# Kernel tuning notes

Measured on AMD Instinct MI355X. Metric: run time of the kernel, lower is better.

The kernel has to match this reference:

```python
import jax, jax.numpy as jnp
import numpy as np

C_IN = 128
C_HID = 32
N_HEAD = 4
LN_EPS = 1e-5


def layer_norm(x, w, b):
    mu = jnp.mean(x, axis=-1, keepdims=True)
    var = jnp.mean(jnp.square(x - mu), axis=-1, keepdims=True)
    return (x - mu) * jax.lax.rsqrt(var + LN_EPS) * w + b


def setup_inputs() -> dict:
    key = jax.random.key(0)
    ks = jax.random.split(key, 12)
    B, N = 1, 256
    act = jax.random.normal(ks[0], (B, N, N, C_IN), dtype=jnp.float32)
    mask = jnp.ones((B, N, N), dtype=jnp.float32)
    s_in = 1.0 / np.sqrt(C_IN)
    s_o = 1.0 / np.sqrt(C_HID * N_HEAD)
    return {
        "act": act,
        "mask": mask,
        "ln_w": jnp.ones((C_IN,), jnp.float32),
        "ln_b": jnp.zeros((C_IN,), jnp.float32),
        "w_2d": jax.random.normal(ks[1], (C_IN, N_HEAD), jnp.float32) * s_in,
        "wq": jax.random.normal(ks[2], (C_IN, N_HEAD * C_HID), jnp.float32) * s_in,
        "wk": jax.random.normal(ks[3], (C_IN, N_HEAD * C_HID), jnp.float32) * s_in,
        "wv": jax.random.normal(ks[4], (C_IN, N_HEAD * C_HID), jnp.float32) * s_in,
        "wg": jax.random.normal(ks[5], (C_IN, N_HEAD * C_HID), jnp.float32) * s_in,
        "bg": jnp.ones((N_HEAD * C_HID,), jnp.float32),
        "wo": jax.random.normal(ks[6], (N_HEAD * C_HID, C_IN), jnp.float32) * s_o,
        "bo": jnp.zeros((C_IN,), jnp.float32),
    }


def reference(act, mask, ln_w, ln_b, w_2d, wq, wk, wv, wg, bg, wo, bo):
    B, N = act.shape[0], act.shape[1]
    H, c = N_HEAD, C_HID

    x = layer_norm(act, ln_w, ln_b)                       # [B,I,J,C]

    # mask bias: [B, I, 1, 1, K]
    bias = (1e9 * (mask - 1.0))[:, :, None, None, :]
    # pair bias from projected activations: [B, 1, H, Q, K]
    nb = jnp.einsum("bqkc,ch->bhqk", x, w_2d)[:, None]

    scale = c ** (-0.5)
    q = (x @ wq).reshape(B, N, N, H, c) * scale           # [B,I,Q,H,c]
    k = (x @ wk).reshape(B, N, N, H, c)                   # [B,I,K,H,c]
    v = (x @ wv).reshape(B, N, N, H, c)

    logits = jnp.einsum("biqhc,bikhc->bihqk", q, k) + bias + nb
    a = jax.nn.softmax(logits, axis=-1)                   # [B,I,H,Q,K]
    o = jnp.einsum("bihqk,bikhc->biqhc", a, v)            # [B,I,Q,H,c]

    g = jax.nn.sigmoid(x @ wg + bg).reshape(B, N, N, H, c)
    o = (o * g).reshape(B, N, N, H * c)
    return o @ wo + bo
```

## Files before the change

### kernel.cpp

```cpp
#include <hip/hip_runtime.h>
#include <hip/hip_bf16.h>
#include <math.h>

#define C_IN   128
#define NSEQ   256
#define LN_EPS 1e-5f
#define LOG2E  1.4426950408889634f

typedef __attribute__((ext_vector_type(8))) short bf16x8;
typedef __attribute__((ext_vector_type(4))) float f32x4;

__device__ __forceinline__ short f2bf(float x) {
    unsigned u = __builtin_bit_cast(unsigned, x);
    u = (u + 0x7FFF + ((u >> 16) & 1)) >> 16;
    return (short)u;
}


__global__ __launch_bounds__(256) void prep_kernel(
    const float* __restrict__ wq, const float* __restrict__ wk,
    const float* __restrict__ wv, const float* __restrict__ wg,
    const float* __restrict__ wo, const float* __restrict__ w2d,
    short* __restrict__ wT)
{
    int gid = blockIdx.x * 256 + threadIdx.x;
    if (gid < 5 * 16384) {
        int m = gid >> 14, r = gid & 16383, col = r >> 7, k = r & 127;
        const float* W = (m == 0) ? wq : (m == 1) ? wk : (m == 2) ? wv
                       : (m == 3) ? wg : wo;
        float s = (m == 0) ? (0.17677669529663687f * LOG2E) : 1.0f;
        wT[gid] = f2bf(W[k * 128 + col] * s);
    } else if (gid < 5 * 16384 + 16 * 128) {
        int r = gid - 5 * 16384, col = r >> 7, k = r & 127;
        float v = (col < 4) ? w2d[k * 4 + col] * LOG2E : 0.0f;
        wT[gid] = f2bf(v);
    }
}

__global__ __launch_bounds__(256) void proj_kernel(
    const float* __restrict__ act, const float* __restrict__ ln_w,
    const float* __restrict__ ln_b, const float* __restrict__ bg,
    const short* __restrict__ wT,
    short* __restrict__ q_buf, short* __restrict__ k_buf,
    short* __restrict__ v_buf, float* __restrict__ g_buf,
    float* __restrict__ nb2)
{
    __shared__ float psum[4][64], psq[4][64];
    __shared__ float mu_s[64], rs_s[64];
    __shared__ float lnw_s[128], lnb_s[128];

    const int tid = threadIdx.x;
    const int pbase = blockIdx.x * 64;

    if (tid < 128) { lnw_s[tid] = ln_w[tid]; lnb_s[tid] = ln_b[tid]; }

    {
        int m = tid >> 2, qd = tid & 3;
        const float* row = act + (size_t)(pbase + m) * 128 + qd * 32;
        float a = 0.f, b = 0.f;
        #pragma unroll
        for (int j = 0; j < 8; ++j) {
            float4 t = *(const float4*)(row + j * 4);
            a += t.x + t.y + t.z + t.w;
            b += t.x * t.x + t.y * t.y + t.z * t.z + t.w * t.w;
        }
        psum[qd][m] = a; psq[qd][m] = b;
    }
    __syncthreads();
    if (tid < 64) {
        float a = psum[0][tid] + psum[1][tid] + psum[2][tid] + psum[3][tid];
        float b = psq[0][tid] + psq[1][tid] + psq[2][tid] + psq[3][tid];
        float mu = a * (1.f / 128.f);
        float var = b * (1.f / 128.f) - mu * mu;
        mu_s[tid] = mu; rs_s[tid] = rsqrtf(var + LN_EPS);
    }
    __syncthreads();

    const int w = tid >> 6, l = tid & 63, lr = l & 15, lh = l >> 4;

    bf16x8 af[4][4];
    #pragma unroll
    for (int qt = 0; qt < 4; ++qt) {
        int m = qt * 16 + lr;
        float mu = mu_s[m], rs = rs_s[m];
        const float* rowp = act + (size_t)(pbase + m) * 128 + lh * 8;
        #pragma unroll
        for (int kc = 0; kc < 4; ++kc) {
            float4 a = *(const float4*)(rowp + kc * 32);
            float4 b = *(const float4*)(rowp + kc * 32 + 4);
            int c0 = kc * 32 + lh * 8;
            bf16x8 f;
            f[0] = f2bf((a.x - mu) * rs * lnw_s[c0 + 0] + lnb_s[c0 + 0]);
            f[1] = f2bf((a.y - mu) * rs * lnw_s[c0 + 1] + lnb_s[c0 + 1]);
            f[2] = f2bf((a.z - mu) * rs * lnw_s[c0 + 2] + lnb_s[c0 + 2]);
            f[3] = f2bf((a.w - mu) * rs * lnw_s[c0 + 3] + lnb_s[c0 + 3]);
            f[4] = f2bf((b.x - mu) * rs * lnw_s[c0 + 4] + lnb_s[c0 + 4]);
            f[5] = f2bf((b.y - mu) * rs * lnw_s[c0 + 5] + lnb_s[c0 + 5]);
            f[6] = f2bf((b.z - mu) * rs * lnw_s[c0 + 6] + lnb_s[c0 + 6]);
            f[7] = f2bf((b.w - mu) * rs * lnw_s[c0 + 7] + lnb_s[c0 + 7]);
            af[qt][kc] = f;
        }
    }

    const int nct = (w == 0) ? 9 : 8;
    for (int ct = 0; ct < nct; ++ct) {
        const short* bp = (ct < 8)
            ? (wT + w * 16384 + (ct * 16 + lr) * 128 + lh * 8)
            : (wT + 5 * 16384 + lr * 128 + lh * 8);
        f32x4 z = {0.f, 0.f, 0.f, 0.f};
        f32x4 acc0 = z, acc1 = z, acc2 = z, acc3 = z;
        #pragma unroll
        for (int kc = 0; kc < 4; ++kc) {
            bf16x8 b = *(const bf16x8*)(bp + kc * 32);
            acc0 = __builtin_amdgcn_mfma_f32_16x16x32_bf16(af[0][kc], b, acc0, 0, 0, 0);
            acc1 = __builtin_amdgcn_mfma_f32_16x16x32_bf16(af[1][kc], b, acc1, 0, 0, 0);
            acc2 = __builtin_amdgcn_mfma_f32_16x16x32_bf16(af[2][kc], b, acc2, 0, 0, 0);
            acc3 = __builtin_amdgcn_mfma_f32_16x16x32_bf16(af[3][kc], b, acc3, 0, 0, 0);
        }
        f32x4 acc[4] = {acc0, acc1, acc2, acc3};
        if (ct < 8) {
            int col = ct * 16 + lr;
            if (w == 3) {
                float bgv = bg[col];
                #pragma unroll
                for (int qt = 0; qt < 4; ++qt)
                    #pragma unroll
                    for (int r = 0; r < 4; ++r) {
                        float v = acc[qt][r] + bgv;
                        v = 1.f / (1.f + exp2f(-v * LOG2E));
                        g_buf[(size_t)(pbase + qt * 16 + lh * 4 + r) * 128 + col] = v;
                    }
            } else {
                short* obuf = (w == 0) ? q_buf : (w == 1) ? k_buf : v_buf;
                #pragma unroll
                for (int qt = 0; qt < 4; ++qt)
                    #pragma unroll
                    for (int r = 0; r < 4; ++r)
                        obuf[(size_t)(pbase + qt * 16 + lh * 4 + r) * 128 + col] =
                            f2bf(acc[qt][r]);
            }
        } else {
            int col = lr;
            if (col < 4) {
                #pragma unroll
                for (int qt = 0; qt < 4; ++qt)
                    #pragma unroll
                    for (int r = 0; r < 4; ++r)
                        nb2[(size_t)col * 65536 + pbase + qt * 16 + lh * 4 + r] =
                            acc[qt][r];
            }
        }
    }
}

__global__ __launch_bounds__(256) void attn_kernel(
    const float* __restrict__ mask,
    const short* __restrict__ q_buf, const short* __restrict__ k_buf,
    const short* __restrict__ v_buf, const float* __restrict__ g_buf,
    const float* __restrict__ nb2, short* __restrict__ og_buf)
{
    __shared__ short k_s[256 * 40];
    __shared__ short vt_s[32 * 264];
    __shared__ short p_s[4][64 * 40];
    __shared__ float bias_s[256];

    const int tid = threadIdx.x, bid = blockIdx.x;
    const int i = bid >> 2, h = bid & 3;
    const size_t pb = (size_t)i * 256 * 128 + h * 32;

    {
        const short* kp = k_buf + pb + (size_t)tid * 128;
        const short* vp = v_buf + pb + (size_t)tid * 128;
        bf16x8 kv[4], vv[4];
        #pragma unroll
        for (int j = 0; j < 4; ++j) kv[j] = *(const bf16x8*)(kp + j * 8);
        #pragma unroll
        for (int j = 0; j < 4; ++j) vv[j] = *(const bf16x8*)(vp + j * 8);
        #pragma unroll
        for (int j = 0; j < 4; ++j) *(bf16x8*)&k_s[tid * 40 + j * 8] = kv[j];
        #pragma unroll
        for (int j = 0; j < 4; ++j)
            #pragma unroll
            for (int e = 0; e < 8; ++e)
                vt_s[(j * 8 + e) * 264 + tid] = vv[j][e];
        bias_s[tid] = 1e9f * (mask[i * 256 + tid] - 1.f) * LOG2E;
    }

    const int w = tid >> 6, l = tid & 63, lr = l & 15, lh = l >> 4;
    const int qbase = w * 64;

    bf16x8 qf[4];
    #pragma unroll
    for (int qt = 0; qt < 4; ++qt)
        qf[qt] = *(const bf16x8*)(q_buf + pb +
                    (size_t)(qbase + qt * 16 + lr) * 128 + lh * 8);
    __syncthreads();

    f32x4 z = {0.f, 0.f, 0.f, 0.f};
    f32x4 o[4][2];
    float lsum[4][4];
    #pragma unroll
    for (int qt = 0; qt < 4; ++qt) {
        o[qt][0] = z; o[qt][1] = z;
        #pragma unroll
        for (int r = 0; r < 4; ++r) lsum[qt][r] = 0.f;
    }
    short* pw = &p_s[w][0];

    for (int kk = 0; kk < 256; kk += 32) {
        bf16x8 bk0 = *(const bf16x8*)&k_s[(kk + lr) * 40 + lh * 8];
        bf16x8 bk1 = *(const bf16x8*)&k_s[(kk + 16 + lr) * 40 + lh * 8];
        f32x4 s[4][2];
        #pragma unroll
        for (int qt = 0; qt < 4; ++qt) {
            s[qt][0] = __builtin_amdgcn_mfma_f32_16x16x32_bf16(qf[qt], bk0, z, 0, 0, 0);
            s[qt][1] = __builtin_amdgcn_mfma_f32_16x16x32_bf16(qf[qt], bk1, z, 0, 0, 0);
        }
        float b0 = bias_s[kk + lr], b1 = bias_s[kk + 16 + lr];
        #pragma unroll
        for (int qt = 0; qt < 4; ++qt) {
            int q = qbase + qt * 16 + lh * 4;
            const float* nbp = nb2 + (size_t)h * 65536 + (size_t)q * 256 + kk + lr;
            #pragma unroll
            for (int r = 0; r < 4; ++r) {
                float n0 = nbp[r * 256], n1 = nbp[r * 256 + 16];
                float p0 = exp2f(s[qt][0][r] + b0 + n0);
                float p1 = exp2f(s[qt][1][r] + b1 + n1);
                lsum[qt][r] += p0 + p1;
                pw[(qt * 16 + lh * 4 + r) * 40 + lr]      = f2bf(p0);
                pw[(qt * 16 + lh * 4 + r) * 40 + 16 + lr] = f2bf(p1);
            }
        }
        __syncthreads();
        bf16x8 bv0 = *(const bf16x8*)&vt_s[lr * 264 + kk + lh * 8];
        bf16x8 bv1 = *(const bf16x8*)&vt_s[(16 + lr) * 264 + kk + lh * 8];
        #pragma unroll
        for (int qt = 0; qt < 4; ++qt) {
            bf16x8 ap = *(const bf16x8*)&pw[(qt * 16 + lr) * 40 + lh * 8];
            o[qt][0] = __builtin_amdgcn_mfma_f32_16x16x32_bf16(ap, bv0, o[qt][0], 0, 0, 0);
            o[qt][1] = __builtin_amdgcn_mfma_f32_16x16x32_bf16(ap, bv1, o[qt][1], 0, 0, 0);
        }
        __syncthreads();
    }

    #pragma unroll
    for (int qt = 0; qt < 4; ++qt)
        #pragma unroll
        for (int r = 0; r < 4; ++r) {
            float v = lsum[qt][r];
            v += __shfl_xor(v, 1); v += __shfl_xor(v, 2);
            v += __shfl_xor(v, 4); v += __shfl_xor(v, 8);
            lsum[qt][r] = 1.f / v;
        }

    #pragma unroll
    for (int qt = 0; qt < 4; ++qt)
        #pragma unroll
        for (int ct = 0; ct < 2; ++ct) {
            int c = ct * 16 + lr;
            #pragma unroll
            for (int r = 0; r < 4; ++r) {
                int q = qbase + qt * 16 + lh * 4 + r;
                size_t idx = pb + (size_t)q * 128 + c;
                float gv = g_buf[idx];
                og_buf[idx] = f2bf(o[qt][ct][r] * lsum[qt][r] * gv);
            }
        }
}

__global__ __launch_bounds__(256) void out_kernel(
    const short* __restrict__ og_buf, const short* __restrict__ wT,
    const float* __restrict__ bo, float* __restrict__ out)
{
    const int tid = threadIdx.x;
    const int pbase = blockIdx.x * 64;
    const int w = tid >> 6, l = tid & 63, lr = l & 15, lh = l >> 4;

    bf16x8 af[4][4];
    #pragma unroll
    for (int qt = 0; qt < 4; ++qt) {
        const short* rp = og_buf + (size_t)(pbase + qt * 16 + lr) * 128 + lh * 8;
        #pragma unroll
        for (int kc = 0; kc < 4; ++kc) af[qt][kc] = *(const bf16x8*)(rp + kc * 32);
    }
    const short* wo_t = wT + 4 * 16384;
    f32x4 z = {0.f, 0.f, 0.f, 0.f};
    #pragma unroll
    for (int ct = 0; ct < 2; ++ct) {
        int col = w * 32 + ct * 16 + lr;
        f32x4 acc0 = z, acc1 = z, acc2 = z, acc3 = z;
        #pragma unroll
        for (int kc = 0; kc < 4; ++kc) {
            bf16x8 b = *(const bf16x8*)(wo_t + col * 128 + kc * 32 + lh * 8);
            acc0 = __builtin_amdgcn_mfma_f32_16x16x32_bf16(af[0][kc], b, acc0, 0, 0, 0);
            acc1 = __builtin_amdgcn_mfma_f32_16x16x32_bf16(af[1][kc], b, acc1, 0, 0, 0);
            acc2 = __builtin_amdgcn_mfma_f32_16x16x32_bf16(af[2][kc], b, acc2, 0, 0, 0);
            acc3 = __builtin_amdgcn_mfma_f32_16x16x32_bf16(af[3][kc], b, acc3, 0, 0, 0);
        }
        f32x4 acc[4] = {acc0, acc1, acc2, acc3};
        float bov = bo[col];
        #pragma unroll
        for (int qt = 0; qt < 4; ++qt)
            #pragma unroll
            for (int r = 0; r < 4; ++r)
                out[(size_t)(pbase + qt * 16 + lh * 4 + r) * 128 + col] =
                    acc[qt][r] + bov;
    }
}

extern "C" void kernel_launch(void* const* d_in, const int* in_sizes, int n_in,
                              void* d_out, int out_size, void* d_ws, size_t ws_size,
                              hipStream_t stream) {
    const float* act  = (const float*)d_in[0];
    const float* mask = (const float*)d_in[1];
    const float* ln_w = (const float*)d_in[2];
    const float* ln_b = (const float*)d_in[3];
    const float* w2d  = (const float*)d_in[4];
    const float* wq   = (const float*)d_in[5];
    const float* wk   = (const float*)d_in[6];
    const float* wv   = (const float*)d_in[7];
    const float* wg   = (const float*)d_in[8];
    const float* bg   = (const float*)d_in[9];
    const float* wo   = (const float*)d_in[10];
    const float* bo   = (const float*)d_in[11];
    float* out = (float*)d_out;

    char* ws = (char*)d_ws;
    short* q_buf  = (short*)(ws);
    short* k_buf  = (short*)(ws + 16777216);
    short* v_buf  = (short*)(ws + 2 * 16777216);
    short* og_buf = (short*)(ws + 3 * 16777216);
    float* g_buf  = (float*)(ws + 4 * 16777216);
    float* nb2    = (float*)(ws + 4 * 16777216 + 33554432);
    short* wT     = (short*)(ws + 4 * 16777216 + 33554432 + 1048576);

    prep_kernel<<<328, 256, 0, stream>>>(wq, wk, wv, wg, wo, w2d, wT);
    proj_kernel<<<1024, 256, 0, stream>>>(act, ln_w, ln_b, bg, wT,
                                          q_buf, k_buf, v_buf, g_buf, nb2);
    attn_kernel<<<1024, 256, 0, stream>>>(mask, q_buf, k_buf, v_buf, g_buf,
                                          nb2, og_buf);
    out_kernel<<<1024, 256, 0, stream>>>(og_buf, wT, bo, out);
}
```

Measured before the change: 130.8 us.

## Restructure projection/attention: transposed V, bf16 gate, LDS-staged coalesced stores, no K/V LDS

The projection kernel now handles 32 rows per block across twice as many blocks. Its outputs are staged through LDS so global stores are coalesced, V is written pre-transposed, and the gate is stored as bf16 instead of fp32. The attention kernel drops its K/V LDS staging and per-iteration barriers, reading K and transposed V straight from global memory, and packs probabilities with a hardware bf16 convert. The aim is less memory traffic and fewer syncs, at the cost of more global loads inside the attention inner loop and some gate precision.

```diff
diff --git a/kernel.cpp b/kernel.cpp
--- a/kernel.cpp
+++ b/kernel.cpp
@@ -1,19 +1,20 @@
 #include <hip/hip_runtime.h>
-#include <hip/hip_bf16.h>
 #include <math.h>
 
-#define C_IN   128
-#define NSEQ   256
+#define LOG2E  1.4426950408889634f
 #define LN_EPS 1e-5f
-#define LOG2E  1.4426950408889634f
 
 typedef __attribute__((ext_vector_type(8))) short bf16x8;
 typedef __attribute__((ext_vector_type(4))) float f32x4;
+typedef __attribute__((ext_vector_type(4))) unsigned u32x4;
 
 __device__ __forceinline__ short f2bf(float x) {
     unsigned u = __builtin_bit_cast(unsigned, x);
     u = (u + 0x7FFF + ((u >> 16) & 1)) >> 16;
     return (short)u;
+}
+__device__ __forceinline__ float bf2f(unsigned short b) {
+    return __builtin_bit_cast(float, (unsigned)b << 16);
 }
 
 
@@ -42,45 +43,45 @@
     const float* __restrict__ ln_b, const float* __restrict__ bg,
     const short* __restrict__ wT,
     short* __restrict__ q_buf, short* __restrict__ k_buf,
-    short* __restrict__ v_buf, float* __restrict__ g_buf,
+    short* __restrict__ v_t, short* __restrict__ g_buf,
     float* __restrict__ nb2)
 {
-    __shared__ float psum[4][64], psq[4][64];
-    __shared__ float mu_s[64], rs_s[64];
+    __shared__ short trans[4][32 * 136];
+    __shared__ float mu_s[32], rs_s[32];
     __shared__ float lnw_s[128], lnb_s[128];
 
     const int tid = threadIdx.x;
-    const int pbase = blockIdx.x * 64;
+    const int pbase = blockIdx.x * 32;
+    const int i = pbase >> 8, jb = pbase & 255;
 
     if (tid < 128) { lnw_s[tid] = ln_w[tid]; lnb_s[tid] = ln_b[tid]; }
 
     {
-        int m = tid >> 2, qd = tid & 3;
-        const float* row = act + (size_t)(pbase + m) * 128 + qd * 32;
+        int m = tid >> 3, seg = tid & 7;
+        const float* row = act + (size_t)(pbase + m) * 128 + seg * 16;
         float a = 0.f, b = 0.f;
         #pragma unroll
-        for (int j = 0; j < 8; ++j) {
+        for (int j = 0; j < 4; ++j) {
             float4 t = *(const float4*)(row + j * 4);
             a += t.x + t.y + t.z + t.w;
             b += t.x * t.x + t.y * t.y + t.z * t.z + t.w * t.w;
         }
-        psum[qd][m] = a; psq[qd][m] = b;
+        a += __shfl_xor(a, 1); b += __shfl_xor(b, 1);
+        a += __shfl_xor(a, 2); b += __shfl_xor(b, 2);
+        a += __shfl_xor(a, 4); b += __shfl_xor(b, 4);
+        if (seg == 0) {
+            float mu = a * (1.f / 128.f);
+            float var = b * (1.f / 128.f) - mu * mu;
+            mu_s[m] = mu; rs_s[m] = rsqrtf(var + LN_EPS);
+        }
     }
     __syncthreads();
-    if (tid < 64) {
-        float a = psum[0][tid] + psum[1][tid] + psum[2][tid] + psum[3][tid];
-        float b = psq[0][tid] + psq[1][tid] + psq[2][tid] + psq[3][tid];
-        float mu = a * (1.f / 128.f);
-        float var = b * (1.f / 128.f) - mu * mu;
-        mu_s[tid] = mu; rs_s[tid] = rsqrtf(var + LN_EPS);
-    }
-    __syncthreads();
 
     const int w = tid >> 6, l = tid & 63, lr = l & 15, lh = l >> 4;
 
-    bf16x8 af[4][4];
-    #pragma unroll
-    for (int qt = 0; qt < 4; ++qt) {
+    bf16x8 af[2][4];
+    #pragma unroll
+    for (int qt = 0; qt < 2; ++qt) {
         int m = qt * 16 + lr;
         float mu = mu_s[m], rs = rs_s[m];
         const float* rowp = act + (size_t)(pbase + m) * 128 + lh * 8;
@@ -102,52 +103,72 @@
         }
     }
 
+    short* tw = &trans[w][0];
     const int nct = (w == 0) ? 9 : 8;
     for (int ct = 0; ct < nct; ++ct) {
         const short* bp = (ct < 8)
             ? (wT + w * 16384 + (ct * 16 + lr) * 128 + lh * 8)
             : (wT + 5 * 16384 + lr * 128 + lh * 8);
         f32x4 z = {0.f, 0.f, 0.f, 0.f};
-        f32x4 acc0 = z, acc1 = z, acc2 = z, acc3 = z;
+        f32x4 acc0 = z, acc1 = z;
         #pragma unroll
         for (int kc = 0; kc < 4; ++kc) {
             bf16x8 b = *(const bf16x8*)(bp + kc * 32);
             acc0 = __builtin_amdgcn_mfma_f32_16x16x32_bf16(af[0][kc], b, acc0, 0, 0, 0);
             acc1 = __builtin_amdgcn_mfma_f32_16x16x32_bf16(af[1][kc], b, acc1, 0, 0, 0);
-            acc2 = __builtin_amdgcn_mfma_f32_16x16x32_bf16(af[2][kc], b, acc2, 0, 0, 0);
-            acc3 = __builtin_amdgcn_mfma_f32_16x16x32_bf16(af[3][kc], b, acc3, 0, 0, 0);
-        }
-        f32x4 acc[4] = {acc0, acc1, acc2, acc3};
+        }
         if (ct < 8) {
             int col = ct * 16 + lr;
             if (w == 3) {
                 float bgv = bg[col];
                 #pragma unroll
-                for (int qt = 0; qt < 4; ++qt)
-                    #pragma unroll
-                    for (int r = 0; r < 4; ++r) {
-                        float v = acc[qt][r] + bgv;
-                        v = 1.f / (1.f + exp2f(-v * LOG2E));
-                        g_buf[(size_t)(pbase + qt * 16 + lh * 4 + r) * 128 + col] = v;
-                    }
+                for (int r = 0; r < 4; ++r) {
+                    float v0 = acc0[r] + bgv, v1 = acc1[r] + bgv;
+                    v0 = __builtin_amdgcn_rcpf(1.f + __builtin_amdgcn_exp2f(-v0 * LOG2E));
+                    v1 = __builtin_amdgcn_rcpf(1.f + __builtin_amdgcn_exp2f(-v1 * LOG2E));
+                    tw[(lh * 4 + r) * 136 + col]      = f2bf(v0);
+                    tw[(16 + lh * 4 + r) * 136 + col] = f2bf(v1);
+                }
             } else {
-                short* obuf = (w == 0) ? q_buf : (w == 1) ? k_buf : v_buf;
                 #pragma unroll
-                for (int qt = 0; qt < 4; ++qt)
-                    #pragma unroll
-                    for (int r = 0; r < 4; ++r)
-                        obuf[(size_t)(pbase + qt * 16 + lh * 4 + r) * 128 + col] =
-                            f2bf(acc[qt][r]);
-            }
-        } else {
-            int col = lr;
-            if (col < 4) {
-                #pragma unroll
-                for (int qt = 0; qt < 4; ++qt)
-                    #pragma unroll
-                    for (int r = 0; r < 4; ++r)
-                        nb2[(size_t)col * 65536 + pbase + qt * 16 + lh * 4 + r] =
-                            acc[qt][r];
+                for (int r = 0; r < 4; ++r) {
+                    tw[(lh * 4 + r) * 136 + col]      = f2bf(acc0[r]);
+                    tw[(16 + lh * 4 + r) * 136 + col] = f2bf(acc1[r]);
+                }
+            }
+        } else if (lr < 4) {
+            #pragma unroll
+            for (int r = 0; r < 4; ++r) {
+                nb2[(size_t)lr * 65536 + pbase + lh * 4 + r]      = acc0[r];
+                nb2[(size_t)lr * 65536 + pbase + 16 + lh * 4 + r] = acc1[r];
+            }
+        }
+    }
+
+    if (w != 2) {
+        short* G = (w == 0) ? q_buf : (w == 1) ? k_buf : g_buf;
+        #pragma unroll
+        for (int ch = 0; ch < 8; ++ch) {
+            int row = ch * 4 + lh;
+            bf16x8 vv = *(const bf16x8*)&tw[row * 136 + lr * 8];
+            *(bf16x8*)(G + (size_t)(pbase + row) * 128 + lr * 8) = vv;
+        }
+    } else {
+        #pragma unroll
+        for (int cc = 0; cc < 2; ++cc) {
+            int col = cc * 64 + l;
+            unsigned wv[16];
+            #pragma unroll
+            for (int m = 0; m < 16; ++m) {
+                unsigned lo = (unsigned short)tw[(2 * m) * 136 + col];
+                unsigned hi = (unsigned short)tw[(2 * m + 1) * 136 + col];
+                wv[m] = lo | (hi << 16);
+            }
+            u32x4* dst = (u32x4*)(v_t + ((size_t)i * 128 + col) * 256 + jb);
+            #pragma unroll
+            for (int t = 0; t < 4; ++t) {
+                u32x4 o4 = { wv[4 * t], wv[4 * t + 1], wv[4 * t + 2], wv[4 * t + 3] };
+                dst[t] = o4;
             }
         }
     }
@@ -156,45 +177,31 @@
 __global__ __launch_bounds__(256) void attn_kernel(
     const float* __restrict__ mask,
     const short* __restrict__ q_buf, const short* __restrict__ k_buf,
-    const short* __restrict__ v_buf, const float* __restrict__ g_buf,
+    const short* __restrict__ v_t, const short* __restrict__ g_buf,
     const float* __restrict__ nb2, short* __restrict__ og_buf)
 {
-    __shared__ short k_s[256 * 40];
-    __shared__ short vt_s[32 * 264];
-    __shared__ short p_s[4][64 * 40];
+    __shared__ unsigned p_lds[4][64 * 20];
     __shared__ float bias_s[256];
 
     const int tid = threadIdx.x, bid = blockIdx.x;
     const int i = bid >> 2, h = bid & 3;
-    const size_t pb = (size_t)i * 256 * 128 + h * 32;
-
-    {
-        const short* kp = k_buf + pb + (size_t)tid * 128;
-        const short* vp = v_buf + pb + (size_t)tid * 128;
-        bf16x8 kv[4], vv[4];
-        #pragma unroll
-        for (int j = 0; j < 4; ++j) kv[j] = *(const bf16x8*)(kp + j * 8);
-        #pragma unroll
-        for (int j = 0; j < 4; ++j) vv[j] = *(const bf16x8*)(vp + j * 8);
-        #pragma unroll
-        for (int j = 0; j < 4; ++j) *(bf16x8*)&k_s[tid * 40 + j * 8] = kv[j];
-        #pragma unroll
-        for (int j = 0; j < 4; ++j)
-            #pragma unroll
-            for (int e = 0; e < 8; ++e)
-                vt_s[(j * 8 + e) * 264 + tid] = vv[j][e];
-        bias_s[tid] = 1e9f * (mask[i * 256 + tid] - 1.f) * LOG2E;
-    }
+
+    bias_s[tid] = 1e9f * (mask[i * 256 + tid] - 1.f) * LOG2E;
+    __syncthreads();
 
     const int w = tid >> 6, l = tid & 63, lr = l & 15, lh = l >> 4;
     const int qbase = w * 64;
 
+    const short* qrow = q_buf + ((size_t)(i * 256 + qbase)) * 128 + h * 32;
     bf16x8 qf[4];
     #pragma unroll
     for (int qt = 0; qt < 4; ++qt)
-        qf[qt] = *(const bf16x8*)(q_buf + pb +
-                    (size_t)(qbase + qt * 16 + lr) * 128 + lh * 8);
-    __syncthreads();
+        qf[qt] = *(const bf16x8*)(qrow + (qt * 16 + lr) * 128 + lh * 8);
+
+    const short* krow = k_buf + ((size_t)(i * 256)) * 128 + h * 32 + lh * 8;
+    const short* vrow = v_t + ((size_t)i * 128 + h * 32) * 256;
+    const float* nbbase = nb2 + (size_t)h * 65536 + (size_t)qbase * 256;
+    unsigned* pw = &p_lds[w][0];
 
     f32x4 z = {0.f, 0.f, 0.f, 0.f};
     f32x4 o[4][2];
@@ -205,44 +212,50 @@
         #pragma unroll
         for (int r = 0; r < 4; ++r) lsum[qt][r] = 0.f;
     }
-    short* pw = &p_s[w][0];
 
     for (int kk = 0; kk < 256; kk += 32) {
-        bf16x8 bk0 = *(const bf16x8*)&k_s[(kk + lr) * 40 + lh * 8];
-        bf16x8 bk1 = *(const bf16x8*)&k_s[(kk + 16 + lr) * 40 + lh * 8];
-        f32x4 s[4][2];
+        bf16x8 bk0 = *(const bf16x8*)(krow + (size_t)(kk + lr) * 128);
+        bf16x8 bk1 = *(const bf16x8*)(krow + (size_t)(kk + 16 + lr) * 128);
+        float b0 = bias_s[kk + lr], b1 = bias_s[kk + 16 + lr];
         #pragma unroll
         for (int qt = 0; qt < 4; ++qt) {
-            s[qt][0] = __builtin_amdgcn_mfma_f32_16x16x32_bf16(qf[qt], bk0, z, 0, 0, 0);
-            s[qt][1] = __builtin_amdgcn_mfma_f32_16x16x32_bf16(qf[qt], bk1, z, 0, 0, 0);
-        }
-        float b0 = bias_s[kk + lr], b1 = bias_s[kk + 16 + lr];
+            f32x4 s0 = __builtin_amdgcn_mfma_f32_16x16x32_bf16(qf[qt], bk0, z, 0, 0, 0);
+            f32x4 s1 = __builtin_amdgcn_mfma_f32_16x16x32_bf16(qf[qt], bk1, z, 0, 0, 0);
+            const float* nbp = nbbase + (size_t)(qt * 16 + lh * 4) * 256 + kk + lr;
+            #pragma unroll
+            for (int r = 0; r < 4; ++r) {
+                float p0 = __builtin_amdgcn_exp2f(s0[r] + b0 + nbp[r * 256]);
+                float p1 = __builtin_amdgcn_exp2f(s1[r] + b1 + nbp[r * 256 + 16]);
+                lsum[qt][r] += p0 + p1;
+                unsigned pk;
+                asm("v_cvt_pk_bf16_f32 %0, %1, %2" : "=v"(pk) : "v"(p0), "v"(p1));
+                pw[(qt * 16 + lh * 4 + r) * 20 + lr] = pk;
+            }
+        }
+        const short* vb = vrow + kk + lh * 4;
+        uint2 a0 = *(const uint2*)(vb + (size_t)lr * 256);
+        uint2 c0 = *(const uint2*)(vb + (size_t)lr * 256 + 16);
+        uint2 a1 = *(const uint2*)(vb + (size_t)(16 + lr) * 256);
+        uint2 c1 = *(const uint2*)(vb + (size_t)(16 + lr) * 256 + 16);
+        u32x4 u0 = { __builtin_amdgcn_perm(c0.x, a0.x, 0x05040100),
+                     __builtin_amdgcn_perm(c0.x, a0.x, 0x07060302),
+                     __builtin_amdgcn_perm(c0.y, a0.y, 0x05040100),
+                     __builtin_amdgcn_perm(c0.y, a0.y, 0x07060302) };
+        u32x4 u1 = { __builtin_amdgcn_perm(c1.x, a1.x, 0x05040100),
+                     __builtin_amdgcn_perm(c1.x, a1.x, 0x07060302),
+                     __builtin_amdgcn_perm(c1.y, a1.y, 0x05040100),
+                     __builtin_amdgcn_perm(c1.y, a1.y, 0x07060302) };
+        bf16x8 bv0 = __builtin_bit_cast(bf16x8, u0);
+        bf16x8 bv1 = __builtin_bit_cast(bf16x8, u1);
         #pragma unroll
         for (int qt = 0; qt < 4; ++qt) {
-            int q = qbase + qt * 16 + lh * 4;
-            const float* nbp = nb2 + (size_t)h * 65536 + (size_t)q * 256 + kk + lr;
-            #pragma unroll
-            for (int r = 0; r < 4; ++r) {
-                float n0 = nbp[r * 256], n1 = nbp[r * 256 + 16];
-                float p0 = exp2f(s[qt][0][r] + b0 + n0);
-                float p1 = exp2f(s[qt][1][r] + b1 + n1);
-                lsum[qt][r] += p0 + p1;
-                pw[(qt * 16 + lh * 4 + r) * 40 + lr]      = f2bf(p0);
-                pw[(qt * 16 + lh * 4 + r) * 40 + 16 + lr] = f2bf(p1);
-            }
-        }
-        __syncthreads();
-        bf16x8 bv0 = *(const bf16x8*)&vt_s[lr * 264 + kk + lh * 8];
-        bf16x8 bv1 = *(const bf16x8*)&vt_s[(16 + lr) * 264 + kk + lh * 8];
-        #pragma unroll
-        for (int qt = 0; qt < 4; ++qt) {
-            bf16x8 ap = *(const bf16x8*)&pw[(qt * 16 + lr) * 40 + lh * 8];
-            o[qt][0] = __builtin_amdgcn_mfma_f32_16x16x32_bf16(ap, bv0, o[qt][0], 0, 0, 0);
-            o[qt][1] = __builtin_amdgcn_mfma_f32_16x16x32_bf16(ap, bv1, o[qt][1], 0, 0, 0);
-        }
-        __syncthreads();
-    }
-
+            bf16x8 pa = *(const bf16x8*)(pw + (qt * 16 + lr) * 20 + lh * 4);
+            o[qt][0] = __builtin_amdgcn_mfma_f32_16x16x32_bf16(pa, bv0, o[qt][0], 0, 0, 0);
+            o[qt][1] = __builtin_amdgcn_mfma_f32_16x16x32_bf16(pa, bv1, o[qt][1], 0, 0, 0);
+        }
+    }
+
+    float inv[4][4];
     #pragma unroll
     for (int qt = 0; qt < 4; ++qt)
         #pragma unroll
@@ -250,9 +263,11 @@
             float v = lsum[qt][r];
             v += __shfl_xor(v, 1); v += __shfl_xor(v, 2);
             v += __shfl_xor(v, 4); v += __shfl_xor(v, 8);
-            lsum[qt][r] = 1.f / v;
-        }
-
+            inv[qt][r] = __builtin_amdgcn_rcpf(v);
+        }
+
+    short* ow = (short*)pw;
+    const short* grow = g_buf + ((size_t)(i * 256 + qbase)) * 128 + h * 32;
     #pragma unroll
     for (int qt = 0; qt < 4; ++qt)
         #pragma unroll
@@ -260,12 +275,17 @@
             int c = ct * 16 + lr;
             #pragma unroll
             for (int r = 0; r < 4; ++r) {
-                int q = qbase + qt * 16 + lh * 4 + r;
-                size_t idx = pb + (size_t)q * 128 + c;
-                float gv = g_buf[idx];
-                og_buf[idx] = f2bf(o[qt][ct][r] * lsum[qt][r] * gv);
-            }
-        }
+                int q = qt * 16 + lh * 4 + r;
+                float gf = bf2f((unsigned short)grow[(size_t)q * 128 + c]);
+                ow[q * 40 + c] = f2bf(o[qt][ct][r] * inv[qt][r] * gf);
+            }
+        }
+    short* og_row = og_buf + ((size_t)(i * 256 + qbase)) * 128 + h * 32;
+    #pragma unroll
+    for (int j = 0; j < 4; ++j) {
+        u32x4 t = *(const u32x4*)(ow + l * 40 + j * 8);
+        *(u32x4*)(og_row + (size_t)l * 128 + j * 8) = t;
+    }
 }
 
 __global__ __launch_bounds__(256) void out_kernel(
@@ -328,16 +348,16 @@
     char* ws = (char*)d_ws;
     short* q_buf  = (short*)(ws);
     short* k_buf  = (short*)(ws + 16777216);
-    short* v_buf  = (short*)(ws + 2 * 16777216);
+    short* v_t    = (short*)(ws + 2 * 16777216);
     short* og_buf = (short*)(ws + 3 * 16777216);
-    float* g_buf  = (float*)(ws + 4 * 16777216);
-    float* nb2    = (float*)(ws + 4 * 16777216 + 33554432);
-    short* wT     = (short*)(ws + 4 * 16777216 + 33554432 + 1048576);
+    short* g_buf  = (short*)(ws + 4 * 16777216);
+    float* nb2    = (float*)(ws + 5 * 16777216);
+    short* wT     = (short*)(ws + 5 * 16777216 + 1048576);
 
     prep_kernel<<<328, 256, 0, stream>>>(wq, wk, wv, wg, wo, w2d, wT);
-    proj_kernel<<<1024, 256, 0, stream>>>(act, ln_w, ln_b, bg, wT,
-                                          q_buf, k_buf, v_buf, g_buf, nb2);
-    attn_kernel<<<1024, 256, 0, stream>>>(mask, q_buf, k_buf, v_buf, g_buf,
+    proj_kernel<<<2048, 256, 0, stream>>>(act, ln_w, ln_b, bg, wT,
+                                          q_buf, k_buf, v_t, g_buf, nb2);
+    attn_kernel<<<1024, 256, 0, stream>>>(mask, q_buf, k_buf, v_t, g_buf,
                                           nb2, og_buf);
     out_kernel<<<1024, 256, 0, stream>>>(og_buf, wT, bo, out);
 }
```

After: 135.5 us. 3.6% more time.
